# Kernel optimization log

Measured on AMD Instinct MI355X. Metric: run time of the kernel, lower is better.

The kernel has to match this reference:

```python
import jax, jax.numpy as jnp
import numpy as np

B, T, V, E, H = 64, 1024, 32000, 300, 200
BUDGET = 10
L_SUP, R_SUP = -0.1, 1.1  # HardKuma stretched support


def setup_inputs() -> dict:
    key = jax.random.key(0)
    ks = jax.random.split(key, 12)
    x = jax.random.randint(ks[0], (B, T), 0, V)
    lengths = jax.random.randint(ks[1], (B,), T // 2, T + 1)
    mask = jnp.arange(T)[None, :] < lengths[:, None]  # contiguous prefix mask
    s = 1.0 / np.sqrt(H)
    return {
        "x": x,
        "mask": mask,
        "embed": jax.random.normal(ks[2], (V, E), jnp.float32) * 0.1,
        "Wih_f": jax.random.uniform(ks[3], (4 * H, E), jnp.float32, -s, s),
        "Whh_f": jax.random.uniform(ks[4], (4 * H, H), jnp.float32, -s, s),
        "b_f": jnp.zeros((4 * H,), jnp.float32),
        "Wih_b": jax.random.uniform(ks[5], (4 * H, E), jnp.float32, -s, s),
        "Whh_b": jax.random.uniform(ks[6], (4 * H, H), jnp.float32, -s, s),
        "b_b": jnp.zeros((4 * H,), jnp.float32),
        "Wa": jax.random.normal(ks[7], (1, 2 * H), jnp.float32) * 1e-3,
        "ba": jnp.zeros((1,), jnp.float32),
        "Wb": jax.random.normal(ks[8], (1, 2 * H), jnp.float32) * 1e-3,
        "bb": jnp.zeros((1,), jnp.float32),
    }


def _lstm(xs, mask, Wih, Whh, b, reverse=False):
    """Packed-sequence-equivalent (masked) unidirectional LSTM. xs:(B,T,E), mask:(B,T) bool -> (B,T,H)."""
    Bq = xs.shape[0]
    Hh = Whh.shape[1]

    def step(carry, inp):
        h, c = carry
        xt, mt = inp  # (B,E), (B,) bool
        g = xt @ Wih.T + h @ Whh.T + b  # (B,4H), torch gate order i,f,g,o
        i, f, gg, o = jnp.split(g, 4, axis=-1)
        c_new = jax.nn.sigmoid(f) * c + jax.nn.sigmoid(i) * jnp.tanh(gg)
        h_new = jax.nn.sigmoid(o) * jnp.tanh(c_new)
        m = mt[:, None]
        h = jnp.where(m, h_new, h)
        c = jnp.where(m, c_new, c)
        return (h, c), jnp.where(m, h, 0.0)  # padded outputs are zero (pack/pad behavior)

    h0 = jnp.zeros((Bq, Hh), xs.dtype)
    (_, _), ys = jax.lax.scan(step, (h0, h0), (jnp.swapaxes(xs, 0, 1), jnp.swapaxes(mask, 0, 1)), reverse=reverse)
    return jnp.swapaxes(ys, 0, 1)


def _kuma_mean(a, b):
    # E[Kuma(a,b)] = b * Beta(1 + 1/a, b), via lgamma for stability
    one_p_inv_a = 1.0 + 1.0 / a
    lbeta = jax.lax.lgamma(one_p_inv_a) + jax.lax.lgamma(b) - jax.lax.lgamma(one_p_inv_a + b)
    return b * jnp.exp(lbeta)


def _forward(x, mask, embed, Wih_f, Whh_f, b_f, Wih_b, Whh_b, b_b, Wa, ba, Wb, bb):
    maskf = mask.astype(jnp.float32)
    lengths = mask.sum(1)  # (B,)
    emb = embed[x]  # (B,T,E); dropout is identity in eval mode
    hf = _lstm(emb, mask, Wih_f, Whh_f, b_f, reverse=False)
    hb = _lstm(emb, mask, Wih_b, Whh_b, b_b, reverse=True)
    h = jnp.concatenate([hf, hb], axis=-1)  # (B,T,2H)
    hs = h / 0.01
    a = jnp.clip(jax.nn.softplus(hs @ Wa.T + ba), 1e-6, 100.0)  # (B,T,1)
    bk = jnp.clip(jax.nn.softplus(hs @ Wb.T + bb), 1e-6, 100.0)
    # HardKuma mean: stretch Kuma mean to support then rectify to [0,1]
    mean = jnp.clip(L_SUP + (R_SUP - L_SUP) * _kuma_mean(a, bk), 0.0, 1.0)
    z_probs = mean[..., 0] * maskf  # zero beyond each length (B,T)
    # per-example budget: k_b = round(budget/100 * len_b) (round-half-even, matches torch.round)
    k = jnp.round((BUDGET / 100.0) * lengths.astype(jnp.float32)).astype(jnp.int32)
    # batched variable-k top-k: rank each position by descending prob, keep rank < k
    order = jnp.argsort(-z_probs, axis=1)
    ranks = jnp.argsort(order, axis=1)  # rank of each position (0 = largest)
    sel = (ranks < k[:, None]) & (z_probs > 0)  # matches z_probs>0 after scatter-zeroing
    z = sel.astype(jnp.float32)
    return jnp.where(mask, z, 0.0)


def reference(x, mask, embed, Wih_f, Whh_f, b_f, Wih_b, Whh_b, b_b, Wa, ba, Wb, bb):
    return _forward(x, mask, embed, Wih_f, Whh_f, b_f, Wih_b, Whh_b, b_b, Wa, ba, Wb, bb)
```

## Files before the change

kernel.cpp:

```cpp
#include <hip/hip_runtime.h>
#include <math.h>

#define Bsz 64
#define Tsz 1024
#define Esz 300
#define Hsz 200
#define Gsz 800
#define NTOK (Bsz*Tsz)
#define WPAD 6400

#define FMA4(A_, W_, H_) do { \
  (A_).x = fmaf((W_).x, (H_), (A_).x); \
  (A_).y = fmaf((W_).y, (H_), (A_).y); \
  (A_).z = fmaf((W_).z, (H_), (A_).z); \
  (A_).w = fmaf((W_).w, (H_), (A_).w); } while (0)


__global__ __launch_bounds__(256) void k_lengths(const void* __restrict__ mraw,
                                                 int* __restrict__ lens) {
  __shared__ int red[256];
  const unsigned char* mb = (const unsigned char*)mraw;
  const int isbool = (mb[1] != 0);
  int b = blockIdx.x, tid = threadIdx.x;
  int s = 0;
  if (isbool) {
    const unsigned char* row = mb + (size_t)b * Tsz;
    for (int i = tid; i < Tsz; i += 256) s += (row[i] != 0);
  } else {
    const int* row = (const int*)mraw + (size_t)b * Tsz;
    for (int i = tid; i < Tsz; i += 256) s += (row[i] != 0);
  }
  red[tid] = s; __syncthreads();
  for (int off = 128; off; off >>= 1) {
    if (tid < off) red[tid] += red[tid + off];
    __syncthreads();
  }
  if (tid == 0) lens[b] = red[0];
}

__global__ __launch_bounds__(256) void k_transpose(const float* __restrict__ Whh,
                                                   float* __restrict__ WhhT) {
  int idx = blockIdx.x * 256 + threadIdx.x;
  if (idx >= Gsz * Hsz) return;
  int r = idx / Hsz, j = idx - r * Hsz;
  int rp = 4 * (r % Hsz) + r / Hsz;
  WhhT[(size_t)j * Gsz + rp] = Whh[idx];
}

#define BM 64
#define BN 160
#define BK 20
__global__ __launch_bounds__(256) void k_gemm(const int* __restrict__ x,
                                              const float* __restrict__ embed,
                                              const float* __restrict__ Wf,
                                              const float* __restrict__ biasf,
                                              const float* __restrict__ Wb_,
                                              const float* __restrict__ biasb,
                                              float* __restrict__ Pf,
                                              float* __restrict__ Pb,
                                              int t0f, int t0b, int tcShift) {
  __shared__ __align__(16) float As[BK][BM];
  __shared__ __align__(16) float Bs[BK][BN];
  __shared__ int toks[BM];
  const int revz = blockIdx.z;
  const float* __restrict__ W    = revz ? Wb_  : Wf;
  const float* __restrict__ bias = revz ? biasb : biasf;
  float* __restrict__ P          = revz ? Pb   : Pf;
  const int t0                   = revz ? t0b  : t0f;
  int tid = threadIdx.x;
  int n0 = blockIdx.x * BM;
  int j0 = blockIdx.y * BN;
  if (tid < BM) {
    int n = n0 + tid;
    toks[tid] = x[((n >> tcShift) << 10) + t0 + (n & ((1 << tcShift) - 1))];
  }
  float acc[8][5];
#pragma unroll
  for (int i = 0; i < 8; i++)
#pragma unroll
    for (int j = 0; j < 5; j++) acc[i][j] = 0.f;
  int rg = tid >> 5;
  int cg = tid & 31;
  for (int k0 = 0; k0 < Esz; k0 += BK) {
    __syncthreads();
    for (int idx = tid; idx < BM * 5; idx += 256) {
      int r = idx / 5, q = idx % 5;
      const float4 v = *reinterpret_cast<const float4*>(
          embed + (size_t)toks[r] * Esz + k0 + q * 4);
      As[q * 4 + 0][r] = v.x; As[q * 4 + 1][r] = v.y;
      As[q * 4 + 2][r] = v.z; As[q * 4 + 3][r] = v.w;
    }
    for (int idx = tid; idx < BN * 5; idx += 256) {
      int j = idx / 5, q = idx % 5;
      int colg = j0 + j;
      int srcRow = (colg & 3) * Hsz + (colg >> 2);
      const float4 v = *reinterpret_cast<const float4*>(
          W + (size_t)srcRow * Esz + k0 + q * 4);
      Bs[q * 4 + 0][j] = v.x; Bs[q * 4 + 1][j] = v.y;
      Bs[q * 4 + 2][j] = v.z; Bs[q * 4 + 3][j] = v.w;
    }
    __syncthreads();
#pragma unroll
    for (int kk = 0; kk < BK; ++kk) {
      float4 a0 = *reinterpret_cast<const float4*>(&As[kk][rg * 8]);
      float4 a1 = *reinterpret_cast<const float4*>(&As[kk][rg * 8 + 4]);
      float a[8] = {a0.x, a0.y, a0.z, a0.w, a1.x, a1.y, a1.z, a1.w};
      float bv[5];
#pragma unroll
      for (int j = 0; j < 5; j++) bv[j] = Bs[kk][cg + 32 * j];
#pragma unroll
      for (int i = 0; i < 8; i++)
#pragma unroll
        for (int j = 0; j < 5; j++) acc[i][j] = fmaf(a[i], bv[j], acc[i][j]);
    }
  }
#pragma unroll
  for (int j = 0; j < 5; j++) {
    int col = j0 + cg + 32 * j;
    float bb = bias[(col & 3) * Hsz + (col >> 2)];
#pragma unroll
    for (int i = 0; i < 8; i++) {
      int n = n0 + rg * 8 + i;
      P[(size_t)n * Gsz + col] = acc[i][j] + bb;
    }
  }
}

#define BM2 128
__global__ __launch_bounds__(512, 2) void k_fused(
    const float* __restrict__ Pf, const float* __restrict__ Pb,
    const float* __restrict__ WhhTf, const float* __restrict__ WhhTb,
    const int* __restrict__ lens,
    const float* __restrict__ Wa, const float* __restrict__ Wb,
    float* __restrict__ hcF, float* __restrict__ hcB,
    float* __restrict__ zaf, float* __restrict__ zbf,
    float* __restrict__ zab, float* __restrict__ zbb,
    int t0f, int t0b, int TC, int tcShift, int init,
    const int* __restrict__ x, const float* __restrict__ embed,
    const float* __restrict__ Wihf, const float* __restrict__ bf,
    const float* __restrict__ Wihb, const float* __restrict__ bb_,
    float* __restrict__ PfN, float* __restrict__ PbN,
    int t0fN, int t0bN, int gemmValid) {
  __shared__ __align__(16) float h[Hsz];
  __shared__ __align__(16) float4 part[1000];
  __shared__ __align__(16) float4 wlds[9000];
  __shared__ float redA[2][8], redB[2][8];
  int bid = blockIdx.x, tid = threadIdx.x;

  if (bid >= 128) {
    if (!gemmValid) return;
    float* As = reinterpret_cast<float*>(wlds);
    float* Bs = As + BK * BM2;
    int*  toks = reinterpret_cast<int*>(Bs + BK * BN);
    int gid = bid - 128;
    int dir = gid / 640;
    int rem = gid - dir * 640;
    int gy = rem / 128;
    int gx = rem - gy * 128;
    const float* __restrict__ W    = dir ? Wihb : Wihf;
    const float* __restrict__ bias = dir ? bb_  : bf;
    float* __restrict__ P          = dir ? PbN  : PfN;
    const int t0                   = dir ? t0bN : t0fN;
    int n0 = gx * BM2;
    int j0 = gy * BN;
    if (tid < BM2) {
      int n = n0 + tid;
      toks[tid] = x[((n >> tcShift) << 10) + t0 + (n & ((1 << tcShift) - 1))];
    }
    float acc[8][5];
#pragma unroll
    for (int i = 0; i < 8; i++)
#pragma unroll
      for (int j = 0; j < 5; j++) acc[i][j] = 0.f;
    int rg = tid >> 5;
    int cg = tid & 31;
    for (int k0 = 0; k0 < Esz; k0 += BK) {
      __syncthreads();
      for (int idx = tid; idx < BM2 * 5; idx += 512) {
        int r = idx / 5, q = idx % 5;
        const float4 v = *reinterpret_cast<const float4*>(
            embed + (size_t)toks[r] * Esz + k0 + q * 4);
        As[(q * 4 + 0) * BM2 + r] = v.x; As[(q * 4 + 1) * BM2 + r] = v.y;
        As[(q * 4 + 2) * BM2 + r] = v.z; As[(q * 4 + 3) * BM2 + r] = v.w;
      }
      for (int idx = tid; idx < BN * 5; idx += 512) {
        int j = idx / 5, q = idx % 5;
        int colg = j0 + j;
        int srcRow = (colg & 3) * Hsz + (colg >> 2);
        const float4 v = *reinterpret_cast<const float4*>(
            W + (size_t)srcRow * Esz + k0 + q * 4);
        Bs[(q * 4 + 0) * BN + j] = v.x; Bs[(q * 4 + 1) * BN + j] = v.y;
        Bs[(q * 4 + 2) * BN + j] = v.z; Bs[(q * 4 + 3) * BN + j] = v.w;
      }
      __syncthreads();
#pragma unroll
      for (int kk = 0; kk < BK; ++kk) {
        float4 a0 = *reinterpret_cast<const float4*>(&As[kk * BM2 + rg * 8]);
        float4 a1 = *reinterpret_cast<const float4*>(&As[kk * BM2 + rg * 8 + 4]);
        float a[8] = {a0.x, a0.y, a0.z, a0.w, a1.x, a1.y, a1.z, a1.w};
        float bv[5];
#pragma unroll
        for (int j = 0; j < 5; j++) bv[j] = Bs[kk * BN + cg + 32 * j];
#pragma unroll
        for (int i = 0; i < 8; i++)
#pragma unroll
          for (int j = 0; j < 5; j++) acc[i][j] = fmaf(a[i], bv[j], acc[i][j]);
      }
    }
#pragma unroll
    for (int j = 0; j < 5; j++) {
      int col = j0 + cg + 32 * j;
      float bb = bias[(col & 3) * Hsz + (col >> 2)];
#pragma unroll
      for (int i = 0; i < 8; i++) {
        int n = n0 + rg * 8 + i;
        P[(size_t)n * Gsz + col] = acc[i][j] + bb;
      }
    }
    return;
  }

  int rev = bid >> 6;
  int b = bid & 63;
  int len = lens[b];
  const float* P    = rev ? Pb : Pf;
  const float* WhhT = rev ? WhhTb : WhhTf;
  float* hcb = (rev ? hcB : hcF) + (size_t)b * 2 * Hsz;
  float* za  = rev ? zab : zaf;
  float* zb  = rev ? zbb : zbf;
  int t0 = rev ? t0b : t0f;
  float wa = 0.f, wb = 0.f, c0 = 0.f;
  if (tid < Hsz) {
    h[tid] = init ? 0.f : hcb[tid];
    c0     = init ? 0.f : hcb[Hsz + tid];
    int off = rev ? Hsz : 0;
    wa = Wa[off + tid]; wb = Wb[off + tid];
  }
  const int worker = (tid < 500);
  int col = 0, gk = 0;
  if (worker) { col = tid % 100; gk = tid / 100; }
  const int hbase = gk * 40;
  const float4* __restrict__ wp4 =
      reinterpret_cast<const float4*>(WhhT) + (size_t)hbase * 200 + 2 * col;

  float4 wreg[40];
  if (worker) {
#pragma unroll
    for (int q = 0; q < 40; q++) wreg[q] = wp4[(q >> 1) * 200 + (q & 1)];
#pragma unroll
    for (int i = 0; i < 18; i++)
      wlds[i * 500 + tid] = wp4[((40 + i) >> 1) * 200 + ((40 + i) & 1)];
  }
  __syncthreads();

  int lo = t0;
  int hi = t0 + TC; if (len < hi) hi = len;
  int nsteps = hi - lo; if (nsteps < 0) nsteps = 0;

  for (int s = 0; s < nsteps; ++s) {
    int t = rev ? (hi - 1 - s) : (lo + s);
    const float4* __restrict__ Prow4 = reinterpret_cast<const float4*>(
        P + ((size_t)b * TC + (t - t0)) * Gsz);
    if (worker) {
      float4 rbuf[8];
#pragma unroll
      for (int q = 0; q < 8; q++)
        rbuf[q] = wp4[((58 + q) >> 1) * 200 + ((58 + q) & 1)];
      float4 acc0, acc1;
      if (gk == 0) { acc0 = Prow4[2 * col]; acc1 = Prow4[2 * col + 1]; }
      else {
        acc0.x = acc0.y = acc0.z = acc0.w = 0.f;
        acc1.x = acc1.y = acc1.z = acc1.w = 0.f;
      }
#pragma unroll
      for (int u = 0; u < 20; u++) {
        float hj = h[hbase + u];
        FMA4(acc0, wreg[2 * u], hj);
        FMA4(acc1, wreg[2 * u + 1], hj);
      }
#pragma unroll
      for (int i = 0; i < 18; i++) {
        float hj = h[hbase + 20 + (i >> 1)];
        float4 wv = wlds[i * 500 + tid];
        if (i & 1) { FMA4(acc1, wv, hj); } else { FMA4(acc0, wv, hj); }
      }
#pragma unroll
      for (int q = 0; q < 14; q++) {
        float4 wv = rbuf[q & 7];
        rbuf[q & 7] = wp4[((66 + q) >> 1) * 200 + ((66 + q) & 1)];
        float hj = h[hbase + ((58 + q) >> 1)];
        if ((58 + q) & 1) { FMA4(acc1, wv, hj); } else { FMA4(acc0, wv, hj); }
      }
#pragma unroll
      for (int q = 14; q < 22; q++) {
        float4 wv = rbuf[q & 7];
        float hj = h[hbase + ((58 + q) >> 1)];
        if ((58 + q) & 1) { FMA4(acc1, wv, hj); } else { FMA4(acc0, wv, hj); }
      }
      part[gk * 200 + 2 * col]     = acc0;
      part[gk * 200 + 2 * col + 1] = acc1;
    }
    __syncthreads();
    float pa = 0.f, pb = 0.f;
    if (tid < Hsz) {
      float4 p0 = part[tid],       p1 = part[200 + tid], p2 = part[400 + tid];
      float4 p3 = part[600 + tid], p4 = part[800 + tid];
      float gi = p0.x + p1.x + p2.x + p3.x + p4.x;
      float gf = p0.y + p1.y + p2.y + p3.y + p4.y;
      float gc = p0.z + p1.z + p2.z + p3.z + p4.z;
      float go = p0.w + p1.w + p2.w + p3.w + p4.w;
      float ig = 1.f / (1.f + expf(-gi));
      float fg = 1.f / (1.f + expf(-gf));
      float gt = tanhf(gc);
      float og = 1.f / (1.f + expf(-go));
      float cn = fmaf(fg, c0, ig * gt);
      float hn = og * tanhf(cn);
      c0 = cn; h[tid] = hn;
      pa = hn * wa; pb = hn * wb;
    }
#pragma unroll
    for (int off = 32; off; off >>= 1) {
      pa += __shfl_down(pa, off);
      pb += __shfl_down(pb, off);
    }
    if ((tid & 63) == 0) { redA[s & 1][tid >> 6] = pa; redB[s & 1][tid >> 6] = pb; }
    __syncthreads();
    if (tid == 0) {
      float sa = 0.f, sb = 0.f;
#pragma unroll
      for (int w = 0; w < 8; ++w) { sa += redA[s & 1][w]; sb += redB[s & 1][w]; }
      za[(size_t)b * Tsz + t] = sa;
      zb[(size_t)b * Tsz + t] = sb;
    }
  }
  if (tid < Hsz) { hcb[tid] = h[tid]; hcb[Hsz + tid] = c0; }
}

__global__ __launch_bounds__(256) void k_head(const float* __restrict__ zaf,
                                              const float* __restrict__ zbf,
                                              const float* __restrict__ zab,
                                              const float* __restrict__ zbb,
                                              const int* __restrict__ lens,
                                              const float* __restrict__ ba,
                                              const float* __restrict__ bb,
                                              float* __restrict__ zp) {
  int n = blockIdx.x * 256 + threadIdx.x;
  if (n >= NTOK) return;
  int b = n >> 10, t = n & 1023;
  if (t >= lens[b]) { zp[n] = 0.f; return; }
  double av = ((double)zaf[n] + (double)zab[n]) * 100.0 + (double)ba[0];
  double bv = ((double)zbf[n] + (double)zbb[n]) * 100.0 + (double)bb[0];
  double a  = av > 0.0 ? av + log1p(exp(-av)) : log1p(exp(av));
  double bk = bv > 0.0 ? bv + log1p(exp(-bv)) : log1p(exp(bv));
  a  = fmin(fmax(a, 1e-6), 100.0);
  bk = fmin(fmax(bk, 1e-6), 100.0);
  double ia = 1.0 + 1.0 / a;
  double lb = lgamma(ia) + lgamma(bk) - lgamma(ia + bk);
  double mean = bk * exp(lb);
  mean = -0.1 + 1.2 * mean;
  mean = fmin(fmax(mean, 0.0), 1.0);
  zp[n] = (float)mean;
}

__global__ __launch_bounds__(256) void k_select(const float* __restrict__ zp,
                                                const int* __restrict__ lens,
                                                float* __restrict__ out) {
  __shared__ float zv[Tsz];
  __shared__ float wbv[4];
  __shared__ int wbi[4];
  __shared__ int stop;
  int b = blockIdx.x, tid = threadIdx.x;
  const float* row = zp + (size_t)b * Tsz;
  for (int i = tid; i < Tsz; i += 256) zv[i] = row[i];
  if (tid == 0) stop = 0;
  int len = lens[b];
  int k = (int)rintf(0.1f * (float)len);
  __syncthreads();
  for (int it = 0; it < k; ++it) {
    float bvl = -1.f; int bil = 0;
#pragma unroll
    for (int s = 0; s < 4; s++) {
      int i = tid * 4 + s;
      float v = zv[i];
      if (v > bvl) { bvl = v; bil = i; }
    }
    for (int off = 32; off; off >>= 1) {
      float ov = __shfl_down(bvl, off);
      int   oi = __shfl_down(bil, off);
      if (ov > bvl || (ov == bvl && oi < bil)) { bvl = ov; bil = oi; }
    }
    int w = tid >> 6;
    if ((tid & 63) == 0) { wbv[w] = bvl; wbi[w] = bil; }
    __syncthreads();
    if (tid == 0) {
      float fb = wbv[0]; int fi = wbi[0];
      for (int q = 1; q < 4; q++)
        if (wbv[q] > fb || (wbv[q] == fb && wbi[q] < fi)) { fb = wbv[q]; fi = wbi[q]; }
      if (fb <= 0.f) stop = 1;
      else { out[(size_t)b * Tsz + fi] = 1.0f; zv[fi] = -1e30f; }
    }
    __syncthreads();
    if (stop) break;
  }
}

extern "C" void kernel_launch(void* const* d_in, const int* in_sizes, int n_in,
                              void* d_out, int out_size, void* d_ws, size_t ws_size,
                              hipStream_t stream) {
  const int*   x      = (const int*)d_in[0];
  const void*  mask   = d_in[1];
  const float* embed  = (const float*)d_in[2];
  const float* Wih_f  = (const float*)d_in[3];
  const float* Whh_f  = (const float*)d_in[4];
  const float* b_f    = (const float*)d_in[5];
  const float* Wih_b  = (const float*)d_in[6];
  const float* Whh_b  = (const float*)d_in[7];
  const float* b_b    = (const float*)d_in[8];
  const float* Wa     = (const float*)d_in[9];
  const float* ba     = (const float*)d_in[10];
  const float* Wb     = (const float*)d_in[11];
  const float* bb     = (const float*)d_in[12];
  float* out = (float*)d_out;

  size_t fixedBytes = (5 * (size_t)NTOK + 2 * (size_t)Bsz * 2 * Hsz +
                       2 * ((size_t)Hsz * Gsz + WPAD)) * sizeof(float) +
                      Bsz * sizeof(int) + 1024;
  const int TCo = 256;
  size_t chunkFlO = (size_t)Bsz * TCo * Gsz;
  size_t needOverlap = fixedBytes + 4 * chunkFlO * sizeof(float);
  int overlap = (ws_size >= needOverlap);

  int TC = TCo, tcShift = 8, nP = 4;
  if (!overlap) {
    const int cand[5] = {256, 128, 64, 32, 16};
    for (int i = 0; i < 5; i++) {
      size_t need = fixedBytes + 2 * (size_t)Bsz * cand[i] * Gsz * sizeof(float);
      if (need <= ws_size) { TC = cand[i]; break; }
    }
    tcShift = 31 - __builtin_clz((unsigned)TC);
    nP = 2;
  }
  size_t chunkFl = (size_t)Bsz * TC * Gsz;

  float* Pbase = (float*)d_ws;
  float* PfA[2], *PbA[2];
  if (overlap) {
    PfA[0] = Pbase;               PfA[1] = Pbase + chunkFl;
    PbA[0] = Pbase + 2 * chunkFl; PbA[1] = Pbase + 3 * chunkFl;
  } else {
    PfA[0] = PfA[1] = Pbase;
    PbA[0] = PbA[1] = Pbase + chunkFl;
  }
  float* rest  = Pbase + nP * chunkFl;
  float* zaf   = rest;
  float* zbf   = zaf + NTOK;
  float* zab   = zbf + NTOK;
  float* zbb   = zab + NTOK;
  float* zp    = zbb + NTOK;
  float* hcF   = zp + NTOK;
  float* hcB   = hcF + (size_t)Bsz * 2 * Hsz;
  float* WhhTf = hcB + (size_t)Bsz * 2 * Hsz;
  float* WhhTb = WhhTf + (size_t)Hsz * Gsz + WPAD;
  int*   lens  = (int*)(WhhTb + (size_t)Hsz * Gsz + WPAD);

  k_lengths<<<Bsz, 256, 0, stream>>>(mask, lens);
  const int tgrid = (Gsz * Hsz + 255) / 256;
  k_transpose<<<tgrid, 256, 0, stream>>>(Whh_f, WhhTf);
  k_transpose<<<tgrid, 256, 0, stream>>>(Whh_b, WhhTb);

  int nch = Tsz / TC;
  if (overlap) {
    dim3 gg((Bsz * TC) / BM, Gsz / BN, 2);
    k_gemm<<<gg, 256, 0, stream>>>(x, embed, Wih_f, b_f, Wih_b, b_b,
                                   PfA[0], PbA[0], 0, (nch - 1) * TC, tcShift);
    for (int i = 0; i < nch; ++i) {
      int gv = (i < nch - 1);
      int grid = 128 + (gv ? 1280 : 0);
      k_fused<<<grid, 512, 0, stream>>>(
          PfA[i & 1], PbA[i & 1], WhhTf, WhhTb, lens, Wa, Wb, hcF, hcB,
          zaf, zbf, zab, zbb, i * TC, (nch - 1 - i) * TC, TC, tcShift, i == 0,
          x, embed, Wih_f, b_f, Wih_b, b_b,
          PfA[(i + 1) & 1], PbA[(i + 1) & 1],
          (i + 1) * TC, (nch - 2 - i) * TC, gv);
    }
  } else {
    dim3 gg((Bsz * TC) / BM, Gsz / BN, 2);
    for (int i = 0; i < nch; ++i) {
      k_gemm<<<gg, 256, 0, stream>>>(x, embed, Wih_f, b_f, Wih_b, b_b,
                                     PfA[0], PbA[0], i * TC,
                                     (nch - 1 - i) * TC, tcShift);
      k_fused<<<128, 512, 0, stream>>>(
          PfA[0], PbA[0], WhhTf, WhhTb, lens, Wa, Wb, hcF, hcB,
          zaf, zbf, zab, zbb, i * TC, (nch - 1 - i) * TC, TC, tcShift, i == 0,
          x, embed, Wih_f, b_f, Wih_b, b_b, PfA[0], PbA[0], 0, 0, 0);
    }
  }

  k_head<<<NTOK / 256, 256, 0, stream>>>(zaf, zbf, zab, zbb, lens, ba, bb, zp);

  (void)hipMemsetAsync(d_out, 0, (size_t)out_size * sizeof(float), stream);
  k_select<<<Bsz, 256, 0, stream>>>(zp, lens, out);
}
```

Baseline: 3.588 ms.

## Use a smaller first time chunk to shorten the unoverlapped input GEMM prologue

```diff
diff --git a/kernel.cpp b/kernel.cpp
--- a/kernel.cpp
+++ b/kernel.cpp
@@ -135,12 +135,12 @@
     float* __restrict__ hcF, float* __restrict__ hcB,
     float* __restrict__ zaf, float* __restrict__ zbf,
     float* __restrict__ zab, float* __restrict__ zbb,
-    int t0f, int t0b, int TC, int tcShift, int init,
+    int t0f, int t0b, int TC, int init,
     const int* __restrict__ x, const float* __restrict__ embed,
     const float* __restrict__ Wihf, const float* __restrict__ bf,
     const float* __restrict__ Wihb, const float* __restrict__ bb_,
     float* __restrict__ PfN, float* __restrict__ PbN,
-    int t0fN, int t0bN, int gemmValid) {
+    int t0fN, int t0bN, int tcShiftN, int nGx, int gemmValid) {
   __shared__ __align__(16) float h[Hsz];
   __shared__ __align__(16) float4 part[1000];
   __shared__ __align__(16) float4 wlds[9000];
@@ -153,10 +153,11 @@
     float* Bs = As + BK * BM2;
     int*  toks = reinterpret_cast<int*>(Bs + BK * BN);
     int gid = bid - 128;
-    int dir = gid / 640;
-    int rem = gid - dir * 640;
-    int gy = rem / 128;
-    int gx = rem - gy * 128;
+    int bpd = nGx * 5;
+    int dir = gid / bpd;
+    int rem = gid - dir * bpd;
+    int gy = rem / nGx;
+    int gx = rem - gy * nGx;
     const float* __restrict__ W    = dir ? Wihb : Wihf;
     const float* __restrict__ bias = dir ? bb_  : bf;
     float* __restrict__ P          = dir ? PbN  : PfN;
@@ -165,7 +166,7 @@
     int j0 = gy * BN;
     if (tid < BM2) {
       int n = n0 + tid;
-      toks[tid] = x[((n >> tcShift) << 10) + t0 + (n & ((1 << tcShift) - 1))];
+      toks[tid] = x[((n >> tcShiftN) << 10) + t0 + (n & ((1 << tcShiftN) - 1))];
     }
     float acc[8][5];
 #pragma unroll
@@ -371,7 +372,10 @@
   __shared__ int stop;
   int b = blockIdx.x, tid = threadIdx.x;
   const float* row = zp + (size_t)b * Tsz;
-  for (int i = tid; i < Tsz; i += 256) zv[i] = row[i];
+  for (int i = tid; i < Tsz; i += 256) {
+    zv[i] = row[i];
+    out[(size_t)b * Tsz + i] = 0.f;
+  }
   if (tid == 0) stop = 0;
   int len = lens[b];
   int k = (int)rintf(0.1f * (float)len);
@@ -425,22 +429,21 @@
   size_t fixedBytes = (5 * (size_t)NTOK + 2 * (size_t)Bsz * 2 * Hsz +
                        2 * ((size_t)Hsz * Gsz + WPAD)) * sizeof(float) +
                       Bsz * sizeof(int) + 1024;
-  const int TCo = 256;
-  size_t chunkFlO = (size_t)Bsz * TCo * Gsz;
+  const int TCmax = 256;
+  size_t chunkFlO = (size_t)Bsz * TCmax * Gsz;
   size_t needOverlap = fixedBytes + 4 * chunkFlO * sizeof(float);
   int overlap = (ws_size >= needOverlap);
 
-  int TC = TCo, tcShift = 8, nP = 4;
+  int TC = TCmax, nP = 4;
   if (!overlap) {
     const int cand[5] = {256, 128, 64, 32, 16};
     for (int i = 0; i < 5; i++) {
       size_t need = fixedBytes + 2 * (size_t)Bsz * cand[i] * Gsz * sizeof(float);
       if (need <= ws_size) { TC = cand[i]; break; }
     }
-    tcShift = 31 - __builtin_clz((unsigned)TC);
     nP = 2;
   }
-  size_t chunkFl = (size_t)Bsz * TC * Gsz;
+  size_t chunkFl = (size_t)Bsz * (overlap ? TCmax : TC) * Gsz;
 
   float* Pbase = (float*)d_ws;
   float* PfA[2], *PbA[2];
@@ -468,22 +471,30 @@
   k_transpose<<<tgrid, 256, 0, stream>>>(Whh_f, WhhTf);
   k_transpose<<<tgrid, 256, 0, stream>>>(Whh_b, WhhTb);
 
-  int nch = Tsz / TC;
   if (overlap) {
-    dim3 gg((Bsz * TC) / BM, Gsz / BN, 2);
-    k_gemm<<<gg, 256, 0, stream>>>(x, embed, Wih_f, b_f, Wih_b, b_b,
-                                   PfA[0], PbA[0], 0, (nch - 1) * TC, tcShift);
-    for (int i = 0; i < nch; ++i) {
-      int gv = (i < nch - 1);
-      int grid = 128 + (gv ? 1280 : 0);
+    const int NCH = 5;
+    const int S[NCH]   = {128, 128, 256, 256, 256};
+    const int T0F[NCH] = {0, 128, 256, 512, 768};
+    const int T0B[NCH] = {896, 768, 512, 256, 0};
+    const int SH[NCH]  = {7, 7, 8, 8, 8};
+    dim3 gg0((Bsz * S[0]) / BM, Gsz / BN, 2);
+    k_gemm<<<gg0, 256, 0, stream>>>(x, embed, Wih_f, b_f, Wih_b, b_b,
+                                    PfA[0], PbA[0], T0F[0], T0B[0], SH[0]);
+    for (int i = 0; i < NCH; ++i) {
+      int gv = (i < NCH - 1);
+      int nGx = gv ? (S[i + 1] / 2) : 1;
+      int grid = 128 + (gv ? 2 * nGx * 5 : 0);
       k_fused<<<grid, 512, 0, stream>>>(
           PfA[i & 1], PbA[i & 1], WhhTf, WhhTb, lens, Wa, Wb, hcF, hcB,
-          zaf, zbf, zab, zbb, i * TC, (nch - 1 - i) * TC, TC, tcShift, i == 0,
+          zaf, zbf, zab, zbb, T0F[i], T0B[i], S[i], i == 0,
           x, embed, Wih_f, b_f, Wih_b, b_b,
           PfA[(i + 1) & 1], PbA[(i + 1) & 1],
-          (i + 1) * TC, (nch - 2 - i) * TC, gv);
+          gv ? T0F[i + 1] : 0, gv ? T0B[i + 1] : 0, gv ? SH[i + 1] : 0,
+          nGx, gv);
     }
   } else {
+    int tcShift = 31 - __builtin_clz((unsigned)TC);
+    int nch = Tsz / TC;
     dim3 gg((Bsz * TC) / BM, Gsz / BN, 2);
     for (int i = 0; i < nch; ++i) {
       k_gemm<<<gg, 256, 0, stream>>>(x, embed, Wih_f, b_f, Wih_b, b_b,
@@ -491,13 +502,11 @@
                                      (nch - 1 - i) * TC, tcShift);
       k_fused<<<128, 512, 0, stream>>>(
           PfA[0], PbA[0], WhhTf, WhhTb, lens, Wa, Wb, hcF, hcB,
-          zaf, zbf, zab, zbb, i * TC, (nch - 1 - i) * TC, TC, tcShift, i == 0,
-          x, embed, Wih_f, b_f, Wih_b, b_b, PfA[0], PbA[0], 0, 0, 0);
+          zaf, zbf, zab, zbb, i * TC, (nch - 1 - i) * TC, TC, i == 0,
+          x, embed, Wih_f, b_f, Wih_b, b_b, PfA[0], PbA[0], 0, 0, 0, 1, 0);
     }
   }
 
   k_head<<<NTOK / 256, 256, 0, stream>>>(zaf, zbf, zab, zbb, lens, ba, bb, zp);
-
-  (void)hipMemsetAsync(d_out, 0, (size_t)out_size * sizeof(float), stream);
   k_select<<<Bsz, 256, 0, stream>>>(zp, lens, out);
 }
```

New measurement: 3.599 ms. No clear change (+0.3%).
